# Performance work log

Measured on AMD Instinct MI355X. Metric: run time of the kernel, lower is better.

The kernel has to match this reference:

```python
import jax, jax.numpy as jnp
import numpy as np

ITEMNUM = 100000
TIME_NUM = 512
H = 128
NH = 2
NB = 2
MAXLEN = 200
B = 128
L = 200
NNZ = 1600000
N_INTERVAL = 31
INTERVAL_SCALE = 1.0


def _ln(x, g, b, eps):
    mu = jnp.mean(x, axis=-1, keepdims=True)
    var = jnp.mean((x - mu) ** 2, axis=-1, keepdims=True)
    return (x - mu) * jax.lax.rsqrt(var + eps) * g + b


def _spmm(idx, val, x):
    # sparse [N,N] @ dense [N,H] via gather + segment_sum (COO)
    return jax.ops.segment_sum(val[:, None] * x[idx[1]], idx[0], num_segments=x.shape[0])


def _l2n(x):
    return x / jnp.clip(jnp.linalg.norm(x, axis=-1, keepdims=True), 1e-12)


def _encoder(e, seqs_data, seqs, position, temb, P):
    p = P['pos_emb'][e][position]
    seqs = seqs + p
    temb = temb + p
    gates = jax.nn.sigmoid(temb @ P['gate_W'][e] + P['gate_b'][e])  # [B,L,NB]
    keep = (seqs_data != ITEMNUM - 1)[..., None].astype(seqs.dtype)
    seqs = seqs * keep
    T = seqs.shape[1]
    causal = jnp.triu(jnp.ones((T, T), bool), k=1)  # True above diagonal -> masked
    hd = H // NH
    scale = 1.0 / np.sqrt(hd).astype(np.float32)
    for i in range(NB):
        Q = _ln(seqs, P['aln_g'][e, i], P['aln_b'][e, i], 1e-8)
        q = (Q @ P['qW'][e, i] + P['qb'][e, i]).reshape(-1, T, NH, hd)
        k = (temb @ P['kW'][e, i] + P['kb'][e, i]).reshape(-1, T, NH, hd)
        v = ((seqs + temb) @ P['vW'][e, i] + P['vb'][e, i]).reshape(-1, T, NH, hd)
        scores = jnp.einsum('bqhd,bkhd->bhqk', q, k) * scale
        g = gates[:, :, i]  # per-block time gate [B,T]
        gm = (g[:, :, None] * g[:, None, :])[:, None]  # gate outer product [B,1,T,T]
        gated = jnp.where(causal, -jnp.inf, scores * gm)
        attn = jax.nn.softmax(gated, axis=-1)
        out = jnp.einsum('bhqk,bkhd->bqhd', attn, v).reshape(-1, T, H)
        seqs = Q + out
        seqs = _ln(seqs, P['fln_g'][e, i], P['fln_b'][e, i], 1e-8)
        h = jax.nn.relu(seqs @ P['c1W'][e, i] + P['c1b'][e, i])  # 1x1 conv == linear
        seqs = seqs + h @ P['c2W'][e, i] + P['c2b'][e, i]
        seqs = seqs * keep
    return _ln(seqs, P['lln_g'][e], P['lln_b'][e], 1e-8)


def _forward(embX, embY, embO, time_table, interval_table, adj_val, adjs_val,
             mlp_W1, mlp_b1, mlp_W2, mlp_b2, mlp_lng, mlp_lnb,
             pos_emb, gate_W, gate_b, aln_g, aln_b, qW, kW, vW, qb, kb, vb,
             fln_g, fln_b, c1W, c1b, c2W, c2b, lln_g, lln_b,
             o_seqs, x_seqs, y_seqs, position, x_position, y_position,
             time, x_time, y_time, x_interval_time, y_interval_time, interval_time,
             adj_idx, adjs_idx):
    # 1-layer graph transfer + mean over [orig, propagated]
    eo = _l2n(_spmm(adj_idx, adj_val, embO))
    embO_m = (embO + eo) * 0.5
    ex = _l2n(_spmm(adjs_idx, adjs_val, embX))
    embX_m = (embX + ex) * 0.5
    ey = _l2n(_spmm(adjs_idx, adjs_val, embY))
    embY_m = (embY + ey) * 0.5

    def iv(t):
        idx = jnp.floor(INTERVAL_SCALE * jnp.log2(t.astype(jnp.float32) + 1.0)).astype(jnp.int32)
        return interval_table[idx]

    def mlp(x, i):
        h = jax.nn.relu(x @ mlp_W1[i] + mlp_b1[i]) @ mlp_W2[i] + mlp_b2[i]
        return _ln(h, mlp_lng[i], mlp_lnb[i], 1e-5)

    x_temb = mlp(iv(x_interval_time) + time_table[x_time], 0)
    y_temb = mlp(iv(y_interval_time) + time_table[y_time], 1)
    temb = mlp(iv(interval_time) + time_table[time], 2)

    seq_o = embO_m[o_seqs] + embO[o_seqs]
    seq_x = embX_m[x_seqs] + embX[x_seqs]
    seq_y = embY_m[y_seqs] + embY[y_seqs]

    P = dict(pos_emb=pos_emb, gate_W=gate_W, gate_b=gate_b, aln_g=aln_g, aln_b=aln_b,
             qW=qW, kW=kW, vW=vW, qb=qb, kb=kb, vb=vb, fln_g=fln_g, fln_b=fln_b,
             c1W=c1W, c1b=c1b, c2W=c2W, c2b=c2b, lln_g=lln_g, lln_b=lln_b)
    out_o = _encoder(0, o_seqs, seq_o, position, temb, P)
    out_x = _encoder(1, x_seqs, seq_x, x_position, x_temb, P)
    out_y = _encoder(2, y_seqs, seq_y, y_position, y_temb, P)
    return out_o, out_x, out_y


def setup_inputs():
    key = jax.random.key(0)
    ks = iter(jax.random.split(key, 64))

    def nrm(shape, s=0.02):
        return jax.random.normal(next(ks), shape, dtype=jnp.float32) * s

    d = {}
    for nm in ['o_seqs', 'x_seqs', 'y_seqs']:
        d[nm] = jax.random.randint(next(ks), (B, L), 0, ITEMNUM)
    for nm in ['position', 'x_position', 'y_position']:
        d[nm] = jax.random.randint(next(ks), (B, L), 0, MAXLEN)
    for nm in ['time', 'x_time', 'y_time']:
        d[nm] = jax.random.randint(next(ks), (B, L), 0, TIME_NUM)
    for nm in ['x_interval_time', 'y_interval_time', 'interval_time']:
        d[nm] = jax.random.randint(next(ks), (B, L), 0, 100000)
    d['embX'] = nrm((ITEMNUM, H)).at[ITEMNUM - 1].set(0.0)
    d['embY'] = nrm((ITEMNUM, H)).at[ITEMNUM - 1].set(0.0)
    d['embO'] = nrm((ITEMNUM, H)).at[ITEMNUM - 1].set(0.0)
    d['time_table'] = nrm((TIME_NUM, H)).at[0].set(0.0)
    d['interval_table'] = nrm((N_INTERVAL, H)).at[0].set(0.0)
    d['adj_idx'] = jnp.stack([jax.random.randint(next(ks), (NNZ,), 0, ITEMNUM),
                              jax.random.randint(next(ks), (NNZ,), 0, ITEMNUM)])
    d['adj_val'] = jax.random.uniform(next(ks), (NNZ,), dtype=jnp.float32) / 16.0
    d['adjs_idx'] = jnp.stack([jax.random.randint(next(ks), (NNZ,), 0, ITEMNUM),
                               jax.random.randint(next(ks), (NNZ,), 0, ITEMNUM)])
    d['adjs_val'] = jax.random.uniform(next(ks), (NNZ,), dtype=jnp.float32) / 16.0
    d['mlp_W1'] = nrm((3, H, 512))
    d['mlp_b1'] = jnp.zeros((3, 512), jnp.float32)
    d['mlp_W2'] = nrm((3, 512, H))
    d['mlp_b2'] = jnp.zeros((3, H), jnp.float32)
    d['mlp_lng'] = jnp.ones((3, H), jnp.float32)
    d['mlp_lnb'] = jnp.zeros((3, H), jnp.float32)
    d['pos_emb'] = nrm((3, MAXLEN, H)).at[:, 0].set(0.0)
    d['gate_W'] = nrm((3, H, NB), 0.05)
    d['gate_b'] = jnp.zeros((3, NB), jnp.float32)
    d['aln_g'] = jnp.ones((3, NB, H), jnp.float32)
    d['aln_b'] = jnp.zeros((3, NB, H), jnp.float32)
    for nm in ['qW', 'kW', 'vW', 'c1W', 'c2W']:
        d[nm] = nrm((3, NB, H, H), 0.05)
    for nm in ['qb', 'kb', 'vb', 'c1b', 'c2b']:
        d[nm] = jnp.zeros((3, NB, H), jnp.float32)
    d['fln_g'] = jnp.ones((3, NB, H), jnp.float32)
    d['fln_b'] = jnp.zeros((3, NB, H), jnp.float32)
    d['lln_g'] = jnp.ones((3, H), jnp.float32)
    d['lln_b'] = jnp.zeros((3, H), jnp.float32)
    return d


def reference(o_seqs, x_seqs, y_seqs, position, x_position, y_position, time, x_time, y_time,
              x_interval_time, y_interval_time, interval_time,
              embX, embY, embO, time_table, interval_table, adj_idx, adj_val, adjs_idx, adjs_val,
              mlp_W1, mlp_b1, mlp_W2, mlp_b2, mlp_lng, mlp_lnb,
              pos_emb, gate_W, gate_b, aln_g, aln_b, qW, kW, vW, qb, kb, vb,
              fln_g, fln_b, c1W, c1b, c2W, c2b, lln_g, lln_b):
    return _forward(embX, embY, embO, time_table, interval_table, adj_val, adjs_val,
                    mlp_W1, mlp_b1, mlp_W2, mlp_b2, mlp_lng, mlp_lnb,
                    pos_emb, gate_W, gate_b, aln_g, aln_b, qW, kW, vW, qb, kb, vb,
                    fln_g, fln_b, c1W, c1b, c2W, c2b, lln_g, lln_b,
                    o_seqs, x_seqs, y_seqs, position, x_position, y_position,
                    time, x_time, y_time, x_interval_time, y_interval_time, interval_time,
                    adj_idx, adjs_idx)
```

## Files before the change

### kernel.cpp

```cpp
#include <hip/hip_runtime.h>
#include <math.h>


#define kH 128
#define kT 200
#define kBATCH 128
#define kM (kBATCH * kT)
#define kITEMS 100000
#define kROWS 100000
#define kNNZ 1600000
#define kNEG_INF (-__builtin_huge_valf())
#define kSZ ((size_t)kM * kH)

typedef short s16x8 __attribute__((ext_vector_type(8)));
typedef __bf16 b16x8 __attribute__((ext_vector_type(8)));
typedef float f32x4 __attribute__((ext_vector_type(4)));

static __device__ __forceinline__ short f2bf(float f) {
    unsigned u = __float_as_uint(f);
    unsigned r = (u + 0x7FFFu + ((u >> 16) & 1u)) >> 16;
    return (short)r;
}
static __device__ __forceinline__ f32x4 mfma16(s16x8 a, s16x8 b, f32x4 c) {
    return __builtin_amdgcn_mfma_f32_16x16x32_bf16(
        __builtin_bit_cast(b16x8, a), __builtin_bit_cast(b16x8, b), c, 0, 0, 0);
}

struct P3 { const int* p[3]; };

__global__ void flag_kernel(const int* __restrict__ ids, unsigned char* __restrict__ flags)
{
    flags[ids[blockIdx.x * 256 + threadIdx.x]] = 1;
}

__global__ void rowlist_kernel(const unsigned char* __restrict__ flags,
                               int* __restrict__ rowlist, int* __restrict__ rank,
                               int* __restrict__ nflag)
{
    const int r = blockIdx.x * 256 + threadIdx.x;
    if (r < kROWS && flags[r]) {
        const int pos = atomicAdd(nflag, 1);
        rowlist[pos] = r;
        rank[r] = pos;
    }
}

__global__ void count4_kernel(const int* __restrict__ idx,
                              const unsigned char* __restrict__ flags,
                              int* __restrict__ counts)
{
    const int j4 = (blockIdx.x * 256 + threadIdx.x) * 4;
    if (j4 >= kNNZ) return;
    const int4 r = *reinterpret_cast<const int4*>(&idx[j4]);
    if (flags[r.x]) atomicAdd(&counts[r.x], 1);
    if (flags[r.y]) atomicAdd(&counts[r.y], 1);
    if (flags[r.z]) atomicAdd(&counts[r.z], 1);
    if (flags[r.w]) atomicAdd(&counts[r.w], 1);
}

__global__ __launch_bounds__(256) void scan_pass1(const int* __restrict__ counts,
                                                  int* __restrict__ partial)
{
    const int t = threadIdx.x;
    const int base = blockIdx.x * 1024;
    int s = 0;
#pragma unroll
    for (int i = 0; i < 4; ++i) {
        const int g = base + t + i * 256;
        if (g < kROWS) s += counts[g];
    }
    __shared__ int sd[256];
    sd[t] = s; __syncthreads();
    for (int off = 128; off > 0; off >>= 1) {
        if (t < off) sd[t] += sd[t + off];
        __syncthreads();
    }
    if (t == 0) partial[blockIdx.x] = sd[0];
}

__global__ void scan_pass2(int* __restrict__ partial, int nblk)
{
    const int t = threadIdx.x;
    __shared__ int sd[128];
    const int v = (t < nblk) ? partial[t] : 0;
    sd[t] = v; __syncthreads();
    for (int off = 1; off < 128; off <<= 1) {
        const int a = (t >= off) ? sd[t - off] : 0;
        __syncthreads();
        sd[t] += a;
        __syncthreads();
    }
    if (t < nblk) partial[t] = sd[t] - v;
}

__global__ __launch_bounds__(256) void scan_pass3(const int* __restrict__ counts,
                                                  const int* __restrict__ partial,
                                                  int* __restrict__ offsets,
                                                  int* __restrict__ cursor)
{
    const int t = threadIdx.x;
    const int base = blockIdx.x * 1024;
    int c[4]; int s = 0;
#pragma unroll
    for (int i = 0; i < 4; ++i) {
        const int g = base + t * 4 + i;
        c[i] = (g < kROWS) ? counts[g] : 0;
        s += c[i];
    }
    __shared__ int sd[256];
    sd[t] = s; __syncthreads();
    for (int off = 1; off < 256; off <<= 1) {
        const int a = (t >= off) ? sd[t - off] : 0;
        __syncthreads();
        sd[t] += a;
        __syncthreads();
    }
    int run = partial[blockIdx.x] + sd[t] - s;
#pragma unroll
    for (int i = 0; i < 4; ++i) {
        const int g = base + t * 4 + i;
        if (g < kROWS) {
            offsets[g] = run;
            cursor[g] = run;
            run += c[i];
            if (g == kROWS - 1) offsets[kROWS] = run;
        }
    }
}

__global__ void scatter4_kernel(const int* __restrict__ idx, const float* __restrict__ val,
                                const unsigned char* __restrict__ flags,
                                int* __restrict__ cursor, int2* __restrict__ edges)
{
    const int j4 = (blockIdx.x * 256 + threadIdx.x) * 4;
    if (j4 >= kNNZ) return;
    const int4 r = *reinterpret_cast<const int4*>(&idx[j4]);
    const int4 c = *reinterpret_cast<const int4*>(&idx[kNNZ + j4]);
    const float4 v = *reinterpret_cast<const float4*>(&val[j4]);
    if (flags[r.x]) edges[atomicAdd(&cursor[r.x], 1)] = make_int2(c.x, __float_as_int(v.x));
    if (flags[r.y]) edges[atomicAdd(&cursor[r.y], 1)] = make_int2(c.y, __float_as_int(v.y));
    if (flags[r.z]) edges[atomicAdd(&cursor[r.z], 1)] = make_int2(c.z, __float_as_int(v.z));
    if (flags[r.w]) edges[atomicAdd(&cursor[r.w], 1)] = make_int2(c.w, __float_as_int(v.w));
}

__global__ __launch_bounds__(256) void smooth_kernel(
    const int2* __restrict__ edges, const int* __restrict__ offsets,
    const int* __restrict__ rowlist, const int* __restrict__ nflag,
    const float* __restrict__ emb, float* __restrict__ smc)
{
    const int ri = blockIdx.x * 4 + (threadIdx.x >> 6);
    const int lane = threadIdx.x & 63;
    if (ri >= nflag[0]) return;
    const int row = rowlist[ri];
    const int lo = offsets[row], hi = offsets[row + 1];
    float a0 = 0.f, a1 = 0.f;
    int e = lo;
    for (; e + 4 <= hi; e += 4) {
        const int2 e0 = edges[e],     e1 = edges[e + 1];
        const int2 e2 = edges[e + 2], e3 = edges[e + 3];
        const float2 u0 = *reinterpret_cast<const float2*>(&emb[(size_t)e0.x * kH + 2 * lane]);
        const float2 u1 = *reinterpret_cast<const float2*>(&emb[(size_t)e1.x * kH + 2 * lane]);
        const float2 u2 = *reinterpret_cast<const float2*>(&emb[(size_t)e2.x * kH + 2 * lane]);
        const float2 u3 = *reinterpret_cast<const float2*>(&emb[(size_t)e3.x * kH + 2 * lane]);
        const float v0 = __int_as_float(e0.y), v1 = __int_as_float(e1.y);
        const float v2 = __int_as_float(e2.y), v3 = __int_as_float(e3.y);
        a0 = fmaf(v0, u0.x, a0); a1 = fmaf(v0, u0.y, a1);
        a0 = fmaf(v1, u1.x, a0); a1 = fmaf(v1, u1.y, a1);
        a0 = fmaf(v2, u2.x, a0); a1 = fmaf(v2, u2.y, a1);
        a0 = fmaf(v3, u3.x, a0); a1 = fmaf(v3, u3.y, a1);
    }
    for (; e < hi; ++e) {
        const int2 ed = edges[e];
        const float2 u = *reinterpret_cast<const float2*>(&emb[(size_t)ed.x * kH + 2 * lane]);
        const float v = __int_as_float(ed.y);
        a0 = fmaf(v, u.x, a0); a1 = fmaf(v, u.y, a1);
    }
    float s = a0 * a0 + a1 * a1;
#pragma unroll
    for (int off = 1; off < 64; off <<= 1) s += __shfl_xor(s, off);
    const float inv = 0.5f / fmaxf(sqrtf(s), 1e-12f);
    const float2 us = *reinterpret_cast<const float2*>(&emb[(size_t)row * kH + 2 * lane]);
    float2 o;
    o.x = 1.5f * us.x + a0 * inv;
    o.y = 1.5f * us.y + a1 * inv;
    *reinterpret_cast<float2*>(&smc[(size_t)ri * kH + 2 * lane]) = o;
}

__global__ void gather_kernel(const int* __restrict__ ids, const int* __restrict__ rank,
                              const float* __restrict__ smc, float* __restrict__ seqs)
{
    const int tok = blockIdx.x * 2 + (threadIdx.x >> 7);
    const int c = threadIdx.x & 127;
    seqs[(size_t)tok * kH + c] = smc[(size_t)rank[ids[tok]] * kH + c];
}

__global__ __launch_bounds__(256) void posmg_kernel(
    const int* __restrict__ ids, const int* __restrict__ pos,
    const float* __restrict__ pemb, const float* __restrict__ gW,
    const float* __restrict__ gb,
    float* __restrict__ seqs, float* __restrict__ temb, float* __restrict__ gates,
    const float* __restrict__ alng, const float* __restrict__ alnb,
    float* __restrict__ qbuf)
{
    const int tok = blockIdx.x * 4 + (threadIdx.x >> 6);
    const int lane = threadIdx.x & 63;
    const int pp = pos[tok];
    const float p0 = pemb[(size_t)pp * kH + lane];
    const float p1 = pemb[(size_t)pp * kH + 64 + lane];
    const size_t o = (size_t)tok * kH;
    const float t0 = temb[o + lane] + p0;
    const float t1 = temb[o + 64 + lane] + p1;
    temb[o + lane] = t0;
    temb[o + 64 + lane] = t1;
    const bool keep = ids[tok] != kITEMS - 1;
    const float q0 = keep ? seqs[o + lane] + p0 : 0.f;
    const float q1 = keep ? seqs[o + 64 + lane] + p1 : 0.f;
    seqs[o + lane] = q0;
    seqs[o + 64 + lane] = q1;
#pragma unroll
    for (int i = 0; i < 2; ++i) {
        float g = t0 * gW[lane * 2 + i] + t1 * gW[(64 + lane) * 2 + i];
#pragma unroll
        for (int off = 1; off < 64; off <<= 1) g += __shfl_xor(g, off);
        if (lane == 0) gates[tok * 2 + i] = 1.f / (1.f + expf(-(g + gb[i])));
    }
    float s1 = q0 + q1, s2 = q0 * q0 + q1 * q1;
#pragma unroll
    for (int off = 1; off < 64; off <<= 1) {
        s1 += __shfl_xor(s1, off);
        s2 += __shfl_xor(s2, off);
    }
    const float mean = s1 * (1.f / 128.f);
    float var = s2 * (1.f / 128.f) - mean * mean;
    var = fmaxf(var, 0.f);
    const float rr = rsqrtf(var + 1e-8f);
    qbuf[o + lane]      = (q0 - mean) * rr * alng[lane]      + alnb[lane];
    qbuf[o + 64 + lane] = (q1 - mean) * rr * alng[64 + lane] + alnb[64 + lane];
}

__global__ void build_x_kernel(
    const int* __restrict__ itv, const int* __restrict__ tt,
    const float* __restrict__ interval_table, const float* __restrict__ time_table,
    float* __restrict__ x)
{
    const int tok = blockIdx.x * 2 + (threadIdx.x >> 7);
    const int c = threadIdx.x & 127;
    const int t = itv[tok];
    int idx = (int)floorf(log2f((float)t + 1.0f));
    idx = idx < 0 ? 0 : (idx > 30 ? 30 : idx);
    x[(size_t)tok * kH + c] = interval_table[idx * kH + c] + time_table[(size_t)tt[tok] * kH + c];
}

__global__ void wt_kernel(const float* __restrict__ in, short* __restrict__ out,
                          int kLog, int nLog)
{
    const int i = blockIdx.x * 256 + threadIdx.x;
    const int knLog = kLog + nLog;
    const int b = i >> knLog;
    const int rem = i & ((1 << knLog) - 1);
    const int n = rem >> kLog;
    const int k = rem & ((1 << kLog) - 1);
    out[i] = f2bf(in[((size_t)b << knLog) + ((size_t)k << nLog) + n]);
}

__global__ __launch_bounds__(256) void ln_fln(
    float* __restrict__ seqs_b, const float* __restrict__ flng,
    const float* __restrict__ flnb, int enc0, int i)
{
    const int l = blockIdx.x / (kM / 4);
    const int blk = blockIdx.x % (kM / 4);
    const int wo = (enc0 + l) * 2 + i;
    float* seqs = seqs_b + (size_t)l * kSZ;
    const float* g = flng + wo * kH;
    const float* bb = flnb + wo * kH;
    const int tok = blk * 4 + (threadIdx.x >> 6);
    const int lane = threadIdx.x & 63;
    const float x0 = seqs[(size_t)tok * kH + lane];
    const float x1 = seqs[(size_t)tok * kH + 64 + lane];
    float s1 = x0 + x1, s2 = x0 * x0 + x1 * x1;
#pragma unroll
    for (int off = 1; off < 64; off <<= 1) {
        s1 += __shfl_xor(s1, off);
        s2 += __shfl_xor(s2, off);
    }
    const float mean = s1 * (1.f / 128.f);
    float var = s2 * (1.f / 128.f) - mean * mean;
    var = fmaxf(var, 0.f);
    const float r = rsqrtf(var + 1e-8f);
    seqs[(size_t)tok * kH + lane]      = (x0 - mean) * r * g[lane]      + bb[lane];
    seqs[(size_t)tok * kH + 64 + lane] = (x1 - mean) * r * g[64 + lane] + bb[64 + lane];
}

template <bool ABF>
static __device__ __forceinline__ void gemm_body(
    const void* __restrict__ Av, const float* __restrict__ A2,
    const short* __restrict__ BT, const float* __restrict__ bias,
    float* __restrict__ Craw, short* __restrict__ CrawB,
    float* __restrict__ Cln, const float* __restrict__ resid,
    int N, int K, int relu, const int* __restrict__ mask_ids,
    const float* __restrict__ lnOg, const float* __restrict__ lnOb, float lnOeps)
{
    __shared__ short As[128 * 128];
    __shared__ short Bs[128 * 128];
    const int tid = threadIdx.x;
    const int lane = tid & 63;
    const int w = tid >> 6;
    const int rowBase = blockIdx.y * 128;
    const int colBase = blockIdx.x * 128;
    f32x4 acc[2][8] = {};

    for (int k0 = 0; k0 < K; k0 += 128) {
#pragma unroll
        for (int p = 0; p < 8; ++p) {
            const int chunk = p * 256 + tid;
            const int r = chunk >> 4;
            const int kc = chunk & 15;
            const int byteoff = (r * 256 + kc * 16) ^ ((r & 7) << 4);
            if (ABF) {
                const short* A16 = (const short*)Av;
                const s16x8 v = *reinterpret_cast<const s16x8*>(
                    &A16[(size_t)(rowBase + r) * K + k0 + kc * 8]);
                *reinterpret_cast<s16x8*>(reinterpret_cast<char*>(As) + byteoff) = v;
            } else {
                const float* A = (const float*)Av;
                const float* src = &A[(size_t)(rowBase + r) * K + k0 + kc * 8];
                float4 a0 = *reinterpret_cast<const float4*>(src);
                float4 a1 = *reinterpret_cast<const float4*>(src + 4);
                if (A2) {
                    const float* s2 = &A2[(size_t)(rowBase + r) * K + k0 + kc * 8];
                    float4 b0 = *reinterpret_cast<const float4*>(s2);
                    float4 b1 = *reinterpret_cast<const float4*>(s2 + 4);
                    a0.x += b0.x; a0.y += b0.y; a0.z += b0.z; a0.w += b0.w;
                    a1.x += b1.x; a1.y += b1.y; a1.z += b1.z; a1.w += b1.w;
                }
                s16x8 v;
                v[0] = f2bf(a0.x); v[1] = f2bf(a0.y); v[2] = f2bf(a0.z); v[3] = f2bf(a0.w);
                v[4] = f2bf(a1.x); v[5] = f2bf(a1.y); v[6] = f2bf(a1.z); v[7] = f2bf(a1.w);
                *reinterpret_cast<s16x8*>(reinterpret_cast<char*>(As) + byteoff) = v;
            }
            {
                const s16x8 v = *reinterpret_cast<const s16x8*>(
                    &BT[(size_t)(colBase + r) * K + k0 + kc * 8]);
                *reinterpret_cast<s16x8*>(reinterpret_cast<char*>(Bs) + byteoff) = v;
            }
        }
        __syncthreads();
#pragma unroll
        for (int kk = 0; kk < 4; ++kk) {
            const int kb = (kk * 32 + (lane >> 4) * 8) * 2;
            s16x8 af[2];
#pragma unroll
            for (int mi = 0; mi < 2; ++mi) {
                const int r = w * 32 + mi * 16 + (lane & 15);
                af[mi] = *reinterpret_cast<const s16x8*>(
                    reinterpret_cast<const char*>(As) + ((r * 256 + kb) ^ ((r & 7) << 4)));
            }
#pragma unroll
            for (int nj = 0; nj < 8; ++nj) {
                const int r = nj * 16 + (lane & 15);
                const s16x8 bf = *reinterpret_cast<const s16x8*>(
                    reinterpret_cast<const char*>(Bs) + ((r * 256 + kb) ^ ((r & 7) << 4)));
#pragma unroll
                for (int mi = 0; mi < 2; ++mi)
                    acc[mi][nj] = mfma16(af[mi], bf, acc[mi][nj]);
            }
        }
        __syncthreads();
    }
    const int c = lane & 15, hi = lane >> 4;
#pragma unroll
    for (int mi = 0; mi < 2; ++mi) {
#pragma unroll
        for (int r = 0; r < 4; ++r) {
            const int row = rowBase + w * 32 + mi * 16 + hi * 4 + r;
            float x[8];
#pragma unroll
            for (int nj = 0; nj < 8; ++nj) {
                const int col = colBase + nj * 16 + c;
                x[nj] = acc[mi][nj][r] + bias[col];
                if (relu) x[nj] = fmaxf(x[nj], 0.f);
                if (resid) x[nj] += resid[(size_t)row * N + col];
            }
            if (mask_ids && mask_ids[row] == kITEMS - 1) {
#pragma unroll
                for (int nj = 0; nj < 8; ++nj) x[nj] = 0.f;
            }
            if (Craw) {
#pragma unroll
                for (int nj = 0; nj < 8; ++nj)
                    Craw[(size_t)row * N + colBase + nj * 16 + c] = x[nj];
            }
            if (CrawB) {
#pragma unroll
                for (int nj = 0; nj < 8; ++nj)
                    CrawB[(size_t)row * N + colBase + nj * 16 + c] = f2bf(x[nj]);
            }
            if (lnOg) {
                float s1 = 0.f, s2 = 0.f;
#pragma unroll
                for (int nj = 0; nj < 8; ++nj) { s1 += x[nj]; s2 += x[nj] * x[nj]; }
#pragma unroll
                for (int off = 1; off < 16; off <<= 1) {
                    s1 += __shfl_xor(s1, off);
                    s2 += __shfl_xor(s2, off);
                }
                const float mean = s1 * (1.f / 128.f);
                float var = s2 * (1.f / 128.f) - mean * mean;
                var = fmaxf(var, 0.f);
                const float rr = rsqrtf(var + lnOeps);
#pragma unroll
                for (int nj = 0; nj < 8; ++nj) {
                    const int col = nj * 16 + c;
                    Cln[(size_t)row * kH + col] = (x[nj] - mean) * rr * lnOg[col] + lnOb[col];
                }
            }
        }
    }
}

__global__ __launch_bounds__(256) void gemm_w1(
    const float* __restrict__ A, const short* __restrict__ BT,
    const float* __restrict__ bias, short* __restrict__ C)
{
    gemm_body<false>(A, nullptr, BT, bias, nullptr, C, nullptr, nullptr,
                     512, 128, 1, nullptr, nullptr, nullptr, 0.f);
}

__global__ __launch_bounds__(256) void gemm_w2(
    const short* __restrict__ A, const short* __restrict__ BT,
    const float* __restrict__ bias, float* __restrict__ Cln,
    const float* __restrict__ g, const float* __restrict__ b)
{
    gemm_body<true>(A, nullptr, BT, bias, nullptr, nullptr, Cln, nullptr,
                    128, 512, 0, nullptr, g, b, 1e-5f);
}

__global__ __launch_bounds__(256) void gemm_qkv(
    const float* __restrict__ qbuf_b, const float* __restrict__ temb_b,
    const float* __restrict__ seqs_b, short* __restrict__ qkv16,
    const short* __restrict__ WT, int enc0, int i,
    const float* __restrict__ qb, const float* __restrict__ kb,
    const float* __restrict__ vb)
{
    const int z = blockIdx.z;
    const int l = z / 3, m = z % 3;
    const int wo = (enc0 + l) * 2 + i;
    const float* A  = (m == 0) ? qbuf_b + (size_t)l * kSZ
                    : (m == 1) ? temb_b + (size_t)l * kSZ
                               : seqs_b + (size_t)l * kSZ;
    const float* A2 = (m == 2) ? temb_b + (size_t)l * kSZ : nullptr;
    const short* B  = WT + ((size_t)m * 6 + wo) * 16384;
    const float* bias = ((m == 0) ? qb : (m == 1) ? kb : vb) + wo * kH;
    short* C = qkv16 + (size_t)(l * 3 + m) * kSZ;
    gemm_body<false>(A, A2, B, bias, nullptr, C, nullptr, nullptr,
                     128, 128, 0, nullptr, nullptr, nullptr, 0.f);
}

__global__ __launch_bounds__(256) void gemm_c1(
    const float* __restrict__ seqs_b, short* __restrict__ qkv16,
    const short* __restrict__ c1WT, const float* __restrict__ c1b,
    int enc0, int i)
{
    const int l = blockIdx.z;
    const int wo = (enc0 + l) * 2 + i;
    gemm_body<false>(seqs_b + (size_t)l * kSZ, nullptr,
                     c1WT + (size_t)wo * 16384, c1b + wo * kH,
                     nullptr, qkv16 + (size_t)(l * 3) * kSZ, nullptr, nullptr,
                     128, 128, 1, nullptr, nullptr, nullptr, 0.f);
}

__global__ __launch_bounds__(256) void gemm_c2(
    const short* __restrict__ qkv16, float* __restrict__ seqs_b,
    float* __restrict__ qbuf_b, float* __restrict__ outp,
    const short* __restrict__ c2WT, const float* __restrict__ c2b,
    P3 ids, const float* __restrict__ alng, const float* __restrict__ alnb,
    const float* __restrict__ llng, const float* __restrict__ llnb,
    int enc0, int i)
{
    const int l = blockIdx.z;
    const int genc = enc0 + l;
    const int wo = genc * 2 + i;
    const short* A16 = qkv16 + (size_t)(l * 3) * kSZ;
    float* seqs = seqs_b + (size_t)l * kSZ;
    if (i == 0) {
        gemm_body<true>(A16, nullptr, c2WT + (size_t)wo * 16384, c2b + wo * kH,
                        seqs, nullptr, qbuf_b + (size_t)l * kSZ, seqs,
                        128, 128, 0, ids.p[genc],
                        alng + (genc * 2 + 1) * kH, alnb + (genc * 2 + 1) * kH, 1e-8f);
    } else {
        gemm_body<true>(A16, nullptr, c2WT + (size_t)wo * 16384, c2b + wo * kH,
                        nullptr, nullptr, outp + (size_t)genc * kSZ, seqs,
                        128, 128, 0, ids.p[genc],
                        llng + genc * kH, llnb + genc * kH, 1e-8f);
    }
}

#define aNT 13
#define aVS 232

__global__ __launch_bounds__(256) void attn_mfma(
    const short* __restrict__ qkv16, const float* __restrict__ gates_b,
    const int gi, const float* __restrict__ resid_b, float* __restrict__ out_b)
{
    __shared__ short klds[200 * 64];
    __shared__ short vt[64 * aVS];
    __shared__ short pl[4][16 * aVS];
    __shared__ float glds[224];
    const int bid = (int)blockIdx.x;
    const int l = bid >> 8;
    const int rb = bid & 255;
    const int b = rb >> 1, h = rb & 1, hoff = h * 64;
    const int tid = threadIdx.x, lane = tid & 63, wv = tid >> 6;
    const size_t base = (size_t)b * kT * kH;
    const short* qp16 = qkv16 + (size_t)(l * 3 + 0) * kSZ;
    const short* kp16 = qkv16 + (size_t)(l * 3 + 1) * kSZ;
    const short* vp16 = qkv16 + (size_t)(l * 3 + 2) * kSZ;
    const float* gates = gates_b + (size_t)l * (kM * 2);
    const float* resid = resid_b + (size_t)l * kSZ;
    float* outp = out_b + (size_t)l * kSZ;

    for (int i = tid; i < 1600; i += 256) {
        const int r = i >> 3, c8 = i & 7;
        const s16x8 v = *reinterpret_cast<const s16x8*>(
            &kp16[base + (size_t)r * kH + hoff + c8 * 8]);
        *reinterpret_cast<s16x8*>(reinterpret_cast<char*>(klds) +
            ((r * 128 + c8 * 16) ^ ((r & 7) << 4))) = v;
    }
    for (int i = tid; i < 6400; i += 256) {
        const int k2 = i >> 6, d = i & 63;
        const unsigned v0 = (unsigned short)vp16[base + (size_t)(2 * k2) * kH + hoff + d];
        const unsigned v1 = (unsigned short)vp16[base + (size_t)(2 * k2 + 1) * kH + hoff + d];
        *reinterpret_cast<unsigned*>(reinterpret_cast<char*>(vt) + d * (aVS * 2) + k2 * 4)
            = v0 | (v1 << 16);
    }
    for (int i = tid; i < 1024; i += 256) {
        const int d = i >> 4, k2 = 100 + (i & 15);
        *reinterpret_cast<unsigned*>(reinterpret_cast<char*>(vt) + d * (aVS * 2) + k2 * 4) = 0;
    }
    if (tid < 224) glds[tid] = (tid < 200) ? gates[(b * kT + tid) * 2 + gi] : 0.f;
    for (int i = lane; i < 16 * aVS / 2; i += 64)
        reinterpret_cast<unsigned*>(pl[wv])[i] = 0u;
    __syncthreads();

    const int c = lane & 15, hi = lane >> 4;
    const float scale = 0.125f;

    for (int qt = wv; qt < aNT; qt += 4) {
        const short* s0 = &qp16[base + (size_t)(qt * 16 + c) * kH + hoff + hi * 8];
        const s16x8 aq0 = *reinterpret_cast<const s16x8*>(s0);
        const s16x8 aq1 = *reinterpret_cast<const s16x8*>(s0 + 32);
        f32x4 sc[aNT];
#pragma unroll
        for (int kt = 0; kt < aNT; ++kt) {
            if (kt > qt) continue;
            const int krow = kt * 16 + c;
            const int sw = (krow & 7) << 4;
            const s16x8 bk0 = *reinterpret_cast<const s16x8*>(
                reinterpret_cast<const char*>(klds) + ((krow * 128 + hi * 16) ^ sw));
            const s16x8 bk1 = *reinterpret_cast<const s16x8*>(
                reinterpret_cast<const char*>(klds) + ((krow * 128 + 64 + hi * 16) ^ sw));
            f32x4 s = {0.f, 0.f, 0.f, 0.f};
            s = mfma16(aq0, bk0, s);
            s = mfma16(aq1, bk1, s);
            sc[kt] = s;
        }
        float gq[4], m[4], ps[4];
#pragma unroll
        for (int r = 0; r < 4; ++r) {
            gq[r] = glds[qt * 16 + hi * 4 + r];
            m[r] = kNEG_INF; ps[r] = 0.f;
        }
#pragma unroll
        for (int kt = 0; kt < aNT; ++kt) {
            if (kt > qt) continue;
            const int col = kt * 16 + c;
            const float gk = glds[col] * scale;
#pragma unroll
            for (int r = 0; r < 4; ++r) {
                const int row = qt * 16 + hi * 4 + r;
                const float v = (col <= row && col < 200) ? sc[kt][r] * gq[r] * gk : kNEG_INF;
                sc[kt][r] = v;
                m[r] = fmaxf(m[r], v);
            }
        }
#pragma unroll
        for (int r = 0; r < 4; ++r)
#pragma unroll
            for (int off = 1; off < 16; off <<= 1)
                m[r] = fmaxf(m[r], __shfl_xor(m[r], off));
#pragma unroll
        for (int kt = 0; kt < aNT; ++kt) {
            if (kt > qt) continue;
#pragma unroll
            for (int r = 0; r < 4; ++r) {
                const float p = __expf(sc[kt][r] - m[r]);
                ps[r] += p;
                *reinterpret_cast<short*>(reinterpret_cast<char*>(pl[wv]) +
                    ((hi * 4 + r) * aVS + kt * 16 + c) * 2) = f2bf(p);
            }
        }
#pragma unroll
        for (int r = 0; r < 4; ++r)
#pragma unroll
            for (int off = 1; off < 16; off <<= 1)
                ps[r] += __shfl_xor(ps[r], off);
        f32x4 oacc[4] = {};
        const int nch = (qt + 2) >> 1;
#pragma unroll
        for (int ks = 0; ks < 7; ++ks) {
            if (ks >= nch) continue;
            const s16x8 pa = *reinterpret_cast<const s16x8*>(
                reinterpret_cast<const char*>(pl[wv]) + (c * aVS + ks * 32 + hi * 8) * 2);
#pragma unroll
            for (int n = 0; n < 4; ++n) {
                const s16x8 bv = *reinterpret_cast<const s16x8*>(
                    reinterpret_cast<const char*>(vt) + ((n * 16 + c) * aVS + ks * 32 + hi * 8) * 2);
                oacc[n] = mfma16(pa, bv, oacc[n]);
            }
        }
#pragma unroll
        for (int r = 0; r < 4; ++r) {
            const int row = qt * 16 + hi * 4 + r;
            if (row < 200) {
                const float inv = 1.f / ps[r];
#pragma unroll
                for (int n = 0; n < 4; ++n) {
                    const size_t off = base + (size_t)row * kH + hoff + n * 16 + c;
                    outp[off] = resid[off] + oacc[n][r] * inv;
                }
            }
        }
    }
}

extern "C" void kernel_launch(void* const* d_in, const int* in_sizes, int n_in,
                              void* d_out, int out_size, void* d_ws, size_t ws_size,
                              hipStream_t stream)
{
    const int* ids_i[3] = { (const int*)d_in[0], (const int*)d_in[1], (const int*)d_in[2] };
    const int* pos_i[3] = { (const int*)d_in[3], (const int*)d_in[4], (const int*)d_in[5] };
    const int* tm_i[3]  = { (const int*)d_in[6], (const int*)d_in[7], (const int*)d_in[8] };
    const int* itv_i[3] = { (const int*)d_in[11], (const int*)d_in[9], (const int*)d_in[10] };
    const float* emb_i[3] = { (const float*)d_in[14], (const float*)d_in[12], (const float*)d_in[13] };
    const float* time_table = (const float*)d_in[15];
    const float* interval_table = (const float*)d_in[16];
    const int* adj_idx  = (const int*)d_in[17];
    const float* adj_val = (const float*)d_in[18];
    const int* adjs_idx  = (const int*)d_in[19];
    const float* adjs_val = (const float*)d_in[20];
    const float* mlp_W1 = (const float*)d_in[21];
    const float* mlp_b1 = (const float*)d_in[22];
    const float* mlp_W2 = (const float*)d_in[23];
    const float* mlp_b2 = (const float*)d_in[24];
    const float* mlp_lng = (const float*)d_in[25];
    const float* mlp_lnb = (const float*)d_in[26];
    const float* pos_emb = (const float*)d_in[27];
    const float* gate_W = (const float*)d_in[28];
    const float* gate_b = (const float*)d_in[29];
    const float* aln_g = (const float*)d_in[30];
    const float* aln_b = (const float*)d_in[31];
    const float* qW = (const float*)d_in[32];
    const float* kW = (const float*)d_in[33];
    const float* vW = (const float*)d_in[34];
    const float* c1W = (const float*)d_in[35];
    const float* c2W = (const float*)d_in[36];
    const float* qb = (const float*)d_in[37];
    const float* kb = (const float*)d_in[38];
    const float* vb = (const float*)d_in[39];
    const float* c1b = (const float*)d_in[40];
    const float* c2b = (const float*)d_in[41];
    const float* fln_g = (const float*)d_in[42];
    const float* fln_b = (const float*)d_in[43];
    const float* lln_g = (const float*)d_in[44];
    const float* lln_b = (const float*)d_in[45];

    float* out = (float*)d_out;
    float* ws = (float*)d_ws;

    const size_t HDR = 900000;
    short* WT = (short*)ws;
    int* COUNTS = (int*)(ws + 442368);
    int* OFFS   = COUNTS + kROWS;
    int* CURS   = OFFS + kROWS + 1;
    int* PART   = CURS + kROWS;
    int* ROWLIST = PART + 256;
    int* RANK   = ROWLIST + 25600;
    int* NFLAG  = RANK + kROWS;
    unsigned char* FLAGS = (unsigned char*)(NFLAG + 16);

    const size_t SCRATCH_F = 16307200;
    const size_t needFor = [&](int ne) {
        return (HDR + (size_t)ne * (3 * kSZ + kM * 2) + SCRATCH_F) * 4;
    }(1);
    const size_t need3 = (HDR + (size_t)3 * (3 * kSZ + kM * 2) + SCRATCH_F) * 4;
    if (ws_size < needFor) return;
    const bool merged = ws_size >= need3;
    const int NE = merged ? 3 : 1;

    float* SEQS  = ws + HDR;
    float* TEMB  = SEQS + (size_t)NE * kSZ;
    float* QBUF  = TEMB + (size_t)NE * kSZ;
    float* GATES = QBUF + (size_t)NE * kSZ;
    float* SCRATCH = GATES + (size_t)NE * (kM * 2);
    float* SMC  = SCRATCH;
    float* XBUF = SMC + kSZ;
    short* HID  = (short*)(XBUF + kSZ);
    int2* EDGES = (int2*)(XBUF + kSZ + kM * 256);
    short* QKV16 = (short*)SCRATCH;

    const short* qkvWT = WT;
    const short* c1WT = WT + (size_t)18 * 16384;
    const short* c2WT = WT + (size_t)24 * 16384;
    const short* w1T = WT + (size_t)30 * 16384;
    const short* w2T = w1T + 3 * 65536;

    wt_kernel<<<6 * 16384 / 256, 256, 0, stream>>>(qW, (short*)qkvWT, 7, 7);
    wt_kernel<<<6 * 16384 / 256, 256, 0, stream>>>(kW, (short*)qkvWT + 6 * 16384, 7, 7);
    wt_kernel<<<6 * 16384 / 256, 256, 0, stream>>>(vW, (short*)qkvWT + 12 * 16384, 7, 7);
    wt_kernel<<<6 * 16384 / 256, 256, 0, stream>>>(c1W, (short*)c1WT, 7, 7);
    wt_kernel<<<6 * 16384 / 256, 256, 0, stream>>>(c2W, (short*)c2WT, 7, 7);
    wt_kernel<<<3 * 65536 / 256, 256, 0, stream>>>(mlp_W1, (short*)w1T, 7, 9);
    wt_kernel<<<3 * 65536 / 256, 256, 0, stream>>>(mlp_W2, (short*)w2T, 9, 7);

    const int mi_of[3] = { 2, 0, 1 };
    const int g4 = (kNNZ / 4 + 255) / 256;
    P3 idsPack{ { ids_i[0], ids_i[1], ids_i[2] } };

    auto phaseA = [&](int e, int l) {
        const int* a_idx = (e == 0) ? adj_idx : adjs_idx;
        const float* a_val = (e == 0) ? adj_val : adjs_val;
        float* SEQSl = SEQS + (size_t)l * kSZ;
        float* TEMBl = TEMB + (size_t)l * kSZ;
        float* QBUFl = QBUF + (size_t)l * kSZ;
        float* GATESl = GATES + (size_t)l * (kM * 2);
        hipMemsetAsync(FLAGS, 0, kROWS, stream);
        hipMemsetAsync(COUNTS, 0, kROWS * sizeof(int), stream);
        hipMemsetAsync(NFLAG, 0, sizeof(int), stream);
        flag_kernel<<<kM / 256, 256, 0, stream>>>(ids_i[e], FLAGS);
        rowlist_kernel<<<(kROWS + 255) / 256, 256, 0, stream>>>(FLAGS, ROWLIST, RANK, NFLAG);
        count4_kernel<<<g4, 256, 0, stream>>>(a_idx, FLAGS, COUNTS);
        scan_pass1<<<98, 256, 0, stream>>>(COUNTS, PART);
        scan_pass2<<<1, 128, 0, stream>>>(PART, 98);
        scan_pass3<<<98, 256, 0, stream>>>(COUNTS, PART, OFFS, CURS);
        scatter4_kernel<<<g4, 256, 0, stream>>>(a_idx, a_val, FLAGS, CURS, EDGES);
        smooth_kernel<<<6400, 256, 0, stream>>>(EDGES, OFFS, ROWLIST, NFLAG, emb_i[e], SMC);
        gather_kernel<<<kM / 2, 256, 0, stream>>>(ids_i[e], RANK, SMC, SEQSl);
        build_x_kernel<<<kM / 2, 256, 0, stream>>>(itv_i[e], tm_i[e], interval_table, time_table, XBUF);
        const int mi = mi_of[e];
        gemm_w1<<<dim3(4, kM / 128), 256, 0, stream>>>(
            XBUF, w1T + (size_t)mi * 65536, mlp_b1 + mi * 512, HID);
        gemm_w2<<<dim3(1, kM / 128), 256, 0, stream>>>(
            HID, w2T + (size_t)mi * 65536, mlp_b2 + mi * kH, TEMBl,
            mlp_lng + mi * kH, mlp_lnb + mi * kH);
        posmg_kernel<<<kM / 4, 256, 0, stream>>>(
            ids_i[e], pos_i[e], pos_emb + (size_t)e * kT * kH,
            gate_W + e * kH * 2, gate_b + e * 2, SEQSl, TEMBl, GATESl,
            aln_g + (e * 2) * kH, aln_b + (e * 2) * kH, QBUFl);
    };

    auto phaseB = [&](int enc0, int nenc) {
        for (int i = 0; i < 2; ++i) {
            gemm_qkv<<<dim3(1, kM / 128, 3 * nenc), 256, 0, stream>>>(
                QBUF, TEMB, SEQS, QKV16, qkvWT, enc0, i, qb, kb, vb);
            attn_mfma<<<256 * nenc, 256, 0, stream>>>(QKV16, GATES, i, QBUF, SEQS);
            ln_fln<<<(kM / 4) * nenc, 256, 0, stream>>>(SEQS, fln_g, fln_b, enc0, i);
            gemm_c1<<<dim3(1, kM / 128, nenc), 256, 0, stream>>>(
                SEQS, QKV16, c1WT, c1b, enc0, i);
            gemm_c2<<<dim3(1, kM / 128, nenc), 256, 0, stream>>>(
                QKV16, SEQS, QBUF, out, c2WT, c2b, idsPack,
                aln_g, aln_b, lln_g, lln_b, enc0, i);
        }
    };

    if (merged) {
        for (int e = 0; e < 3; ++e) phaseA(e, e);
        phaseB(0, 3);
    } else {
        for (int e = 0; e < 3; ++e) {
            phaseA(e, 0);
            phaseB(e, 1);
        }
    }
}
```

Baseline: 1.028 ms.

## Stream V in 64-key chunks to shrink attention LDS and merge memsets

The attention kernel no longer stages the full transposed V and a full 200-wide probability row per wave in LDS. It now loads V in 64-key chunks, block-synchronised inside the query-tile loop, recomputes exp for each chunk, and sets launch bounds so three blocks fit per CU. This cuts LDS use to raise occupancy, at the cost of extra barriers, recomputed exponentials and reloading V chunks once per query-tile iteration. Separately, the workspace layout is rearranged so COUNTS, NFLAG and FLAGS are contiguous and can be zeroed with one memset instead of three.

After: 1.068 ms. 3.9% more time.

```diff
diff --git a/kernel.cpp b/kernel.cpp
--- a/kernel.cpp
+++ b/kernel.cpp
@@ -496,15 +496,15 @@
 }
 
 #define aNT 13
-#define aVS 232
-
-__global__ __launch_bounds__(256) void attn_mfma(
+#define aCS 72
+
+__global__ __launch_bounds__(256, 3) void attn_mfma(
     const short* __restrict__ qkv16, const float* __restrict__ gates_b,
     const int gi, const float* __restrict__ resid_b, float* __restrict__ out_b)
 {
     __shared__ short klds[200 * 64];
-    __shared__ short vt[64 * aVS];
-    __shared__ short pl[4][16 * aVS];
+    __shared__ short vt[64 * aCS];
+    __shared__ short pl[4][16 * aCS];
     __shared__ float glds[224];
     const int bid = (int)blockIdx.x;
     const int l = bid >> 8;
@@ -526,107 +526,125 @@
         *reinterpret_cast<s16x8*>(reinterpret_cast<char*>(klds) +
             ((r * 128 + c8 * 16) ^ ((r & 7) << 4))) = v;
     }
-    for (int i = tid; i < 6400; i += 256) {
-        const int k2 = i >> 6, d = i & 63;
-        const unsigned v0 = (unsigned short)vp16[base + (size_t)(2 * k2) * kH + hoff + d];
-        const unsigned v1 = (unsigned short)vp16[base + (size_t)(2 * k2 + 1) * kH + hoff + d];
-        *reinterpret_cast<unsigned*>(reinterpret_cast<char*>(vt) + d * (aVS * 2) + k2 * 4)
-            = v0 | (v1 << 16);
-    }
-    for (int i = tid; i < 1024; i += 256) {
-        const int d = i >> 4, k2 = 100 + (i & 15);
-        *reinterpret_cast<unsigned*>(reinterpret_cast<char*>(vt) + d * (aVS * 2) + k2 * 4) = 0;
-    }
     if (tid < 224) glds[tid] = (tid < 200) ? gates[(b * kT + tid) * 2 + gi] : 0.f;
-    for (int i = lane; i < 16 * aVS / 2; i += 64)
-        reinterpret_cast<unsigned*>(pl[wv])[i] = 0u;
     __syncthreads();
 
     const int c = lane & 15, hi = lane >> 4;
     const float scale = 0.125f;
 
-    for (int qt = wv; qt < aNT; qt += 4) {
-        const short* s0 = &qp16[base + (size_t)(qt * 16 + c) * kH + hoff + hi * 8];
-        const s16x8 aq0 = *reinterpret_cast<const s16x8*>(s0);
-        const s16x8 aq1 = *reinterpret_cast<const s16x8*>(s0 + 32);
+    for (int it = 0; it < 4; ++it) {
+        const int qt = wv + it * 4;
+        const bool active = qt < aNT;
+        s16x8 aq0 = {}, aq1 = {};
         f32x4 sc[aNT];
-#pragma unroll
-        for (int kt = 0; kt < aNT; ++kt) {
-            if (kt > qt) continue;
-            const int krow = kt * 16 + c;
-            const int sw = (krow & 7) << 4;
-            const s16x8 bk0 = *reinterpret_cast<const s16x8*>(
-                reinterpret_cast<const char*>(klds) + ((krow * 128 + hi * 16) ^ sw));
-            const s16x8 bk1 = *reinterpret_cast<const s16x8*>(
-                reinterpret_cast<const char*>(klds) + ((krow * 128 + 64 + hi * 16) ^ sw));
-            f32x4 s = {0.f, 0.f, 0.f, 0.f};
-            s = mfma16(aq0, bk0, s);
-            s = mfma16(aq1, bk1, s);
-            sc[kt] = s;
-        }
-        float gq[4], m[4], ps[4];
-#pragma unroll
-        for (int r = 0; r < 4; ++r) {
-            gq[r] = glds[qt * 16 + hi * 4 + r];
-            m[r] = kNEG_INF; ps[r] = 0.f;
-        }
-#pragma unroll
-        for (int kt = 0; kt < aNT; ++kt) {
-            if (kt > qt) continue;
-            const int col = kt * 16 + c;
-            const float gk = glds[col] * scale;
+        float m[4], ps[4], gq[4];
+        if (active) {
+            const short* s0 = &qp16[base + (size_t)(qt * 16 + c) * kH + hoff + hi * 8];
+            aq0 = *reinterpret_cast<const s16x8*>(s0);
+            aq1 = *reinterpret_cast<const s16x8*>(s0 + 32);
+#pragma unroll
+            for (int kt = 0; kt < aNT; ++kt) {
+                if (kt > qt) continue;
+                const int krow = kt * 16 + c;
+                const int sw = (krow & 7) << 4;
+                const s16x8 bk0 = *reinterpret_cast<const s16x8*>(
+                    reinterpret_cast<const char*>(klds) + ((krow * 128 + hi * 16) ^ sw));
+                const s16x8 bk1 = *reinterpret_cast<const s16x8*>(
+                    reinterpret_cast<const char*>(klds) + ((krow * 128 + 64 + hi * 16) ^ sw));
+                f32x4 s = {0.f, 0.f, 0.f, 0.f};
+                s = mfma16(aq0, bk0, s);
+                s = mfma16(aq1, bk1, s);
+                sc[kt] = s;
+            }
+#pragma unroll
+            for (int r = 0; r < 4; ++r) {
+                gq[r] = glds[qt * 16 + hi * 4 + r];
+                m[r] = kNEG_INF; ps[r] = 0.f;
+            }
+#pragma unroll
+            for (int kt = 0; kt < aNT; ++kt) {
+                if (kt > qt) continue;
+                const int col = kt * 16 + c;
+                const float gk = glds[col] * scale;
+#pragma unroll
+                for (int r = 0; r < 4; ++r) {
+                    const int row = qt * 16 + hi * 4 + r;
+                    const float v = (col <= row && col < 200) ? sc[kt][r] * gq[r] * gk : kNEG_INF;
+                    sc[kt][r] = v;
+                    m[r] = fmaxf(m[r], v);
+                }
+            }
+#pragma unroll
+            for (int r = 0; r < 4; ++r)
+#pragma unroll
+                for (int off = 1; off < 16; off <<= 1)
+                    m[r] = fmaxf(m[r], __shfl_xor(m[r], off));
+#pragma unroll
+            for (int kt = 0; kt < aNT; ++kt) {
+                if (kt > qt) continue;
+#pragma unroll
+                for (int r = 0; r < 4; ++r)
+                    ps[r] += __expf(sc[kt][r] - m[r]);
+            }
+#pragma unroll
+            for (int r = 0; r < 4; ++r)
+#pragma unroll
+                for (int off = 1; off < 16; off <<= 1)
+                    ps[r] += __shfl_xor(ps[r], off);
+        }
+        f32x4 oacc[4] = {};
+        for (int kc = 0; kc <= it; ++kc) {
+            __syncthreads();
+            for (int i = tid; i < 2048; i += 256) {
+                const int k2l = i >> 6, d = i & 63;
+                const int k = kc * 64 + 2 * k2l;
+                unsigned pk = 0;
+                if (k < 200) {
+                    const unsigned v0 = (unsigned short)vp16[base + (size_t)k * kH + hoff + d];
+                    const unsigned v1 = (k + 1 < 200)
+                        ? (unsigned short)vp16[base + (size_t)(k + 1) * kH + hoff + d] : 0u;
+                    pk = v0 | (v1 << 16);
+                }
+                *reinterpret_cast<unsigned*>(reinterpret_cast<char*>(vt)
+                    + d * (aCS * 2) + k2l * 4) = pk;
+            }
+            __syncthreads();
+            if (active && kc * 64 <= qt * 16 + 15) {
+#pragma unroll
+                for (int t4 = 0; t4 < 4; ++t4) {
+                    const int kt = kc * 4 + t4;
+#pragma unroll
+                    for (int r = 0; r < 4; ++r) {
+                        const float p = (kt <= qt) ? __expf(sc[kt][r] - m[r]) : 0.f;
+                        *reinterpret_cast<short*>(reinterpret_cast<char*>(pl[wv]) +
+                            ((hi * 4 + r) * aCS + t4 * 16 + c) * 2) = f2bf(p);
+                    }
+                }
+#pragma unroll
+                for (int ksl = 0; ksl < 2; ++ksl) {
+                    const s16x8 pa = *reinterpret_cast<const s16x8*>(
+                        reinterpret_cast<const char*>(pl[wv]) + (c * aCS + ksl * 32 + hi * 8) * 2);
+#pragma unroll
+                    for (int n = 0; n < 4; ++n) {
+                        const s16x8 bv = *reinterpret_cast<const s16x8*>(
+                            reinterpret_cast<const char*>(vt) +
+                            ((n * 16 + c) * aCS + ksl * 32 + hi * 8) * 2);
+                        oacc[n] = mfma16(pa, bv, oacc[n]);
+                    }
+                }
+            }
+        }
+        if (active) {
 #pragma unroll
             for (int r = 0; r < 4; ++r) {
                 const int row = qt * 16 + hi * 4 + r;
-                const float v = (col <= row && col < 200) ? sc[kt][r] * gq[r] * gk : kNEG_INF;
-                sc[kt][r] = v;
-                m[r] = fmaxf(m[r], v);
-            }
-        }
-#pragma unroll
-        for (int r = 0; r < 4; ++r)
-#pragma unroll
-            for (int off = 1; off < 16; off <<= 1)
-                m[r] = fmaxf(m[r], __shfl_xor(m[r], off));
-#pragma unroll
-        for (int kt = 0; kt < aNT; ++kt) {
-            if (kt > qt) continue;
-#pragma unroll
-            for (int r = 0; r < 4; ++r) {
-                const float p = __expf(sc[kt][r] - m[r]);
-                ps[r] += p;
-                *reinterpret_cast<short*>(reinterpret_cast<char*>(pl[wv]) +
-                    ((hi * 4 + r) * aVS + kt * 16 + c) * 2) = f2bf(p);
-            }
-        }
-#pragma unroll
-        for (int r = 0; r < 4; ++r)
-#pragma unroll
-            for (int off = 1; off < 16; off <<= 1)
-                ps[r] += __shfl_xor(ps[r], off);
-        f32x4 oacc[4] = {};
-        const int nch = (qt + 2) >> 1;
-#pragma unroll
-        for (int ks = 0; ks < 7; ++ks) {
-            if (ks >= nch) continue;
-            const s16x8 pa = *reinterpret_cast<const s16x8*>(
-                reinterpret_cast<const char*>(pl[wv]) + (c * aVS + ks * 32 + hi * 8) * 2);
-#pragma unroll
-            for (int n = 0; n < 4; ++n) {
-                const s16x8 bv = *reinterpret_cast<const s16x8*>(
-                    reinterpret_cast<const char*>(vt) + ((n * 16 + c) * aVS + ks * 32 + hi * 8) * 2);
-                oacc[n] = mfma16(pa, bv, oacc[n]);
-            }
-        }
-#pragma unroll
-        for (int r = 0; r < 4; ++r) {
-            const int row = qt * 16 + hi * 4 + r;
-            if (row < 200) {
-                const float inv = 1.f / ps[r];
-#pragma unroll
-                for (int n = 0; n < 4; ++n) {
-                    const size_t off = base + (size_t)row * kH + hoff + n * 16 + c;
-                    outp[off] = resid[off] + oacc[n][r] * inv;
+                if (row < 200) {
+                    const float inv = 1.f / ps[r];
+#pragma unroll
+                    for (int n = 0; n < 4; ++n) {
+                        const size_t off = base + (size_t)row * kH + hoff + n * 16 + c;
+                        outp[off] = resid[off] + oacc[n][r] * inv;
+                    }
                 }
             }
         }
@@ -680,20 +698,18 @@
     const size_t HDR = 900000;
     short* WT = (short*)ws;
     int* COUNTS = (int*)(ws + 442368);
-    int* OFFS   = COUNTS + kROWS;
+    int* NFLAG  = COUNTS + kROWS;
+    unsigned char* FLAGS = (unsigned char*)(NFLAG + 16);
+    int* OFFS   = (int*)(FLAGS + 100000);
     int* CURS   = OFFS + kROWS + 1;
     int* PART   = CURS + kROWS;
     int* ROWLIST = PART + 256;
     int* RANK   = ROWLIST + 25600;
-    int* NFLAG  = RANK + kROWS;
-    unsigned char* FLAGS = (unsigned char*)(NFLAG + 16);
 
     const size_t SCRATCH_F = 16307200;
-    const size_t needFor = [&](int ne) {
-        return (HDR + (size_t)ne * (3 * kSZ + kM * 2) + SCRATCH_F) * 4;
-    }(1);
+    const size_t need1 = (HDR + (size_t)1 * (3 * kSZ + kM * 2) + SCRATCH_F) * 4;
     const size_t need3 = (HDR + (size_t)3 * (3 * kSZ + kM * 2) + SCRATCH_F) * 4;
-    if (ws_size < needFor) return;
+    if (ws_size < need1) return;
     const bool merged = ws_size >= need3;
     const int NE = merged ? 3 : 1;
 
@@ -733,9 +749,7 @@
         float* TEMBl = TEMB + (size_t)l * kSZ;
         float* QBUFl = QBUF + (size_t)l * kSZ;
         float* GATESl = GATES + (size_t)l * (kM * 2);
-        hipMemsetAsync(FLAGS, 0, kROWS, stream);
-        hipMemsetAsync(COUNTS, 0, kROWS * sizeof(int), stream);
-        hipMemsetAsync(NFLAG, 0, sizeof(int), stream);
+        hipMemsetAsync(COUNTS, 0, kROWS * sizeof(int) + 64 + kROWS, stream);
         flag_kernel<<<kM / 256, 256, 0, stream>>>(ids_i[e], FLAGS);
         rowlist_kernel<<<(kROWS + 255) / 256, 256, 0, stream>>>(FLAGS, ROWLIST, RANK, NFLAG);
         count4_kernel<<<g4, 256, 0, stream>>>(a_idx, FLAGS, COUNTS);
```

## Stream attention P tiles through small LDS chunks and merge workspace memsets

Applied to the files above, without the earlier changes.

The attention kernel no longer writes the full softmax probability row to a wide LDS buffer. It now writes 64-key chunks into a smaller per-wave buffer and runs the PV MFMAs chunk by chunk. This shrinks LDS use and removes the zeroing pass, and launch bounds now request 2 blocks per SM for higher occupancy. The workspace is reordered so COUNTS, NFLAG and FLAGS are contiguous and can be cleared with one memset instead of three, at the cost of extra per-chunk LDS write/read round trips.

New measurement: 935.1 us. -9.0%, faster.

```diff
diff --git a/kernel.cpp b/kernel.cpp
--- a/kernel.cpp
+++ b/kernel.cpp
@@ -497,14 +497,15 @@
 
 #define aNT 13
 #define aVS 232
-
-__global__ __launch_bounds__(256) void attn_mfma(
+#define aPS 72
+
+__global__ __launch_bounds__(256, 2) void attn_mfma(
     const short* __restrict__ qkv16, const float* __restrict__ gates_b,
     const int gi, const float* __restrict__ resid_b, float* __restrict__ out_b)
 {
     __shared__ short klds[200 * 64];
     __shared__ short vt[64 * aVS];
-    __shared__ short pl[4][16 * aVS];
+    __shared__ short pl[4][16 * aPS];
     __shared__ float glds[224];
     const int bid = (int)blockIdx.x;
     const int l = bid >> 8;
@@ -538,8 +539,6 @@
         *reinterpret_cast<unsigned*>(reinterpret_cast<char*>(vt) + d * (aVS * 2) + k2 * 4) = 0;
     }
     if (tid < 224) glds[tid] = (tid < 200) ? gates[(b * kT + tid) * 2 + gi] : 0.f;
-    for (int i = lane; i < 16 * aVS / 2; i += 64)
-        reinterpret_cast<unsigned*>(pl[wv])[i] = 0u;
     __syncthreads();
 
     const int c = lane & 15, hi = lane >> 4;
@@ -588,15 +587,34 @@
 #pragma unroll
             for (int off = 1; off < 16; off <<= 1)
                 m[r] = fmaxf(m[r], __shfl_xor(m[r], off));
-#pragma unroll
-        for (int kt = 0; kt < aNT; ++kt) {
-            if (kt > qt) continue;
-#pragma unroll
-            for (int r = 0; r < 4; ++r) {
-                const float p = __expf(sc[kt][r] - m[r]);
-                ps[r] += p;
-                *reinterpret_cast<short*>(reinterpret_cast<char*>(pl[wv]) +
-                    ((hi * 4 + r) * aVS + kt * 16 + c) * 2) = f2bf(p);
+        f32x4 oacc[4] = {};
+        const int kmax = qt * 16 + 15;
+#pragma unroll
+        for (int kc = 0; kc < 4; ++kc) {
+            if (kc * 64 > kmax) continue;
+#pragma unroll
+            for (int t4 = 0; t4 < 4; ++t4) {
+                const int kt = kc * 4 + t4;
+#pragma unroll
+                for (int r = 0; r < 4; ++r) {
+                    float p = 0.f;
+                    if (kt <= qt) { p = __expf(sc[kt][r] - m[r]); ps[r] += p; }
+                    *reinterpret_cast<short*>(reinterpret_cast<char*>(pl[wv]) +
+                        ((hi * 4 + r) * aPS + t4 * 16 + c) * 2) = f2bf(p);
+                }
+            }
+#pragma unroll
+            for (int ksl = 0; ksl < 2; ++ksl) {
+                if (kc * 64 + ksl * 32 > kmax) continue;
+                const s16x8 pa = *reinterpret_cast<const s16x8*>(
+                    reinterpret_cast<const char*>(pl[wv]) + (c * aPS + ksl * 32 + hi * 8) * 2);
+#pragma unroll
+                for (int n = 0; n < 4; ++n) {
+                    const s16x8 bv = *reinterpret_cast<const s16x8*>(
+                        reinterpret_cast<const char*>(vt) +
+                        ((n * 16 + c) * aVS + kc * 64 + ksl * 32 + hi * 8) * 2);
+                    oacc[n] = mfma16(pa, bv, oacc[n]);
+                }
             }
         }
 #pragma unroll
@@ -604,20 +622,6 @@
 #pragma unroll
             for (int off = 1; off < 16; off <<= 1)
                 ps[r] += __shfl_xor(ps[r], off);
-        f32x4 oacc[4] = {};
-        const int nch = (qt + 2) >> 1;
-#pragma unroll
-        for (int ks = 0; ks < 7; ++ks) {
-            if (ks >= nch) continue;
-            const s16x8 pa = *reinterpret_cast<const s16x8*>(
-                reinterpret_cast<const char*>(pl[wv]) + (c * aVS + ks * 32 + hi * 8) * 2);
-#pragma unroll
-            for (int n = 0; n < 4; ++n) {
-                const s16x8 bv = *reinterpret_cast<const s16x8*>(
-                    reinterpret_cast<const char*>(vt) + ((n * 16 + c) * aVS + ks * 32 + hi * 8) * 2);
-                oacc[n] = mfma16(pa, bv, oacc[n]);
-            }
-        }
 #pragma unroll
         for (int r = 0; r < 4; ++r) {
             const int row = qt * 16 + hi * 4 + r;
@@ -680,20 +684,18 @@
     const size_t HDR = 900000;
     short* WT = (short*)ws;
     int* COUNTS = (int*)(ws + 442368);
-    int* OFFS   = COUNTS + kROWS;
+    int* NFLAG  = COUNTS + kROWS;
+    unsigned char* FLAGS = (unsigned char*)(NFLAG + 16);
+    int* OFFS   = (int*)(FLAGS + 100000);
     int* CURS   = OFFS + kROWS + 1;
     int* PART   = CURS + kROWS;
     int* ROWLIST = PART + 256;
     int* RANK   = ROWLIST + 25600;
-    int* NFLAG  = RANK + kROWS;
-    unsigned char* FLAGS = (unsigned char*)(NFLAG + 16);
 
     const size_t SCRATCH_F = 16307200;
-    const size_t needFor = [&](int ne) {
-        return (HDR + (size_t)ne * (3 * kSZ + kM * 2) + SCRATCH_F) * 4;
-    }(1);
+    const size_t need1 = (HDR + (size_t)1 * (3 * kSZ + kM * 2) + SCRATCH_F) * 4;
     const size_t need3 = (HDR + (size_t)3 * (3 * kSZ + kM * 2) + SCRATCH_F) * 4;
-    if (ws_size < needFor) return;
+    if (ws_size < need1) return;
     const bool merged = ws_size >= need3;
     const int NE = merged ? 3 : 1;
 
@@ -733,9 +735,7 @@
         float* TEMBl = TEMB + (size_t)l * kSZ;
         float* QBUFl = QBUF + (size_t)l * kSZ;
         float* GATESl = GATES + (size_t)l * (kM * 2);
-        hipMemsetAsync(FLAGS, 0, kROWS, stream);
-        hipMemsetAsync(COUNTS, 0, kROWS * sizeof(int), stream);
-        hipMemsetAsync(NFLAG, 0, sizeof(int), stream);
+        hipMemsetAsync(COUNTS, 0, kROWS * sizeof(int) + 64 + kROWS, stream);
         flag_kernel<<<kM / 256, 256, 0, stream>>>(ids_i[e], FLAGS);
         rowlist_kernel<<<(kROWS + 255) / 256, 256, 0, stream>>>(FLAGS, ROWLIST, RANK, NFLAG);
         count4_kernel<<<g4, 256, 0, stream>>>(a_idx, FLAGS, COUNTS);
```
